# Optimization experiments

Hardware: AMD Instinct MI355X
Metric: run time of the kernel (lower is better)

The kernel has to match this reference:

```python
import jax, jax.numpy as jnp
import numpy as np
from jax import lax

NEG = -1e30  # finite stand-in for -inf (avoids NaN grads)
EPS = 1e-7   # keras backend epsilon used by ctc_batch_cost: log(y_pred + eps)

B, T, C, L = 64, 2048, 128, 256


def setup_inputs() -> dict:
    key = jax.random.key(0)
    k1, k2 = jax.random.split(key)
    # labels in [0, C-2]; blank index is C-1 per keras ctc_batch_cost convention
    y_true = jax.random.randint(k1, (B, L), 0, C - 1, dtype=jnp.int32).astype(jnp.int64)
    # y_pred are (unnormalized) per-frame class probabilities, as keras expects softmax output
    y_pred = jax.random.uniform(k2, (B, T, C), dtype=jnp.float32)
    return {"y_true": y_true, "y_pred": y_pred}


def _lse3(a, b, c):
    s = jnp.stack([a, b, c], axis=0)
    m = jnp.max(s, axis=0)
    return m + jnp.log(jnp.sum(jnp.exp(s - m), axis=0))


def _ctc_loss(y_true, y_pred):
    """Faithful jnp version of K.ctc_batch_cost with full input/label lengths."""
    b, t, c = y_pred.shape
    l = y_true.shape[1]
    blank = c - 1
    S = 2 * l + 1

    logp = jnp.log(y_pred + EPS)  # [B,T,C]

    labels = y_true.astype(jnp.int32)
    # extended label sequence: blank, l1, blank, l2, ..., blank  -> [B,S]
    ext = jnp.full((b, S), blank, dtype=jnp.int32).at[:, 1::2].set(labels)
    # gather per-frame log-probs of extended labels -> [B,T,S]
    lp_z = jnp.take_along_axis(logp, jnp.broadcast_to(ext[:, None, :], (b, t, S)), axis=2)

    # skip transition allowed at s if z[s] != blank and z[s] != z[s-2]
    ext_m2 = jnp.concatenate([jnp.full((b, 2), blank, jnp.int32), ext[:, :-2]], axis=1)
    skip = (ext != blank) & (ext != ext_m2) & (jnp.arange(S)[None, :] >= 2)  # [B,S]

    lp_tbs = jnp.transpose(lp_z, (1, 0, 2))  # [T,B,S]

    neg = jnp.full((b, S), NEG, dtype=logp.dtype)
    alpha0 = neg.at[:, 0].set(lp_tbs[0][:, 0]).at[:, 1].set(lp_tbs[0][:, 1])

    neg1 = jnp.full((b, 1), NEG, dtype=logp.dtype)
    neg2 = jnp.full((b, 2), NEG, dtype=logp.dtype)

    def step(alpha, lp_t):
        s1 = jnp.concatenate([neg1, alpha[:, :-1]], axis=1)
        s2 = jnp.where(skip, jnp.concatenate([neg2, alpha[:, :-2]], axis=1), NEG)
        new = _lse3(alpha, s1, s2) + lp_t
        return new, None

    alphaT, _ = lax.scan(step, alpha0, lp_tbs[1:])
    loss = -jnp.logaddexp(alphaT[:, -1], alphaT[:, -2])  # [B]
    return loss[:, None]  # keras ctc_batch_cost returns [B,1]


def reference(y_true, y_pred):
    return _ctc_loss(y_true, y_pred)
```

## Files before the change

### kernel.cpp

```cpp
#include <hip/hip_runtime.h>


#define B_ 64
#define T_ 2048
#define C_ 128
#define L_ 256
#define BLANK_ (C_ - 1)
#define EPSF 1e-7f
#define LN2F 0.69314718055994530942f
#define CH_ 16
#define NCHH_ 64
#define SENT_ (-(1 << 28))

typedef __attribute__((address_space(1))) const void glob_cv;
typedef __attribute__((address_space(3))) void lds_v;

__device__ __forceinline__ void gl2lds16(const float* g, float* l) {
    __builtin_amdgcn_global_load_lds((glob_cv*)g, (lds_v*)l, 16, 0, 0);
}

#define WAIT_VM(n) asm volatile("s_waitcnt vmcnt(" #n ")" ::: "memory")

__device__ __forceinline__ float dpp_shr1_f(float x) {
    return __int_as_float(
        __builtin_amdgcn_update_dpp(0, __float_as_int(x), 0x138, 0xf, 0xf, false));
}
__device__ __forceinline__ int dpp_shr1_i(int x) {
    return __builtin_amdgcn_update_dpp(0, x, 0x138, 0xf, 0xf, false);
}
__device__ __forceinline__ float dpp_shl1_f(float x) {
    return __int_as_float(
        __builtin_amdgcn_update_dpp(0, __float_as_int(x), 0x130, 0xf, 0xf, false));
}
__device__ __forceinline__ int dpp_shl1_i(int x) {
    return __builtin_amdgcn_update_dpp(0, x, 0x130, 0xf, 0xf, false);
}

struct G { float pb, p1, p3, p5, p7; };

__launch_bounds__(128, 1)
__global__ void ctc_loss_kernel(const int* __restrict__ y_true,
                                const float* __restrict__ y_pred,
                                float* __restrict__ out) {
    const int b = blockIdx.x;
    const int tid = threadIdx.x;
    const int w = __builtin_amdgcn_readfirstlane(tid >> 6);
    const int l = tid & 63;

    __shared__ float ring[2][4][CH_ * C_];

    const int* __restrict__ lab = y_true + b * L_;
    const int4 lv = *(const int4*)(lab + 4 * l);
    const int e1 = lv.x, e3 = lv.y, e5 = lv.z, e7 = lv.w;
    const int em1 = (l > 0) ? lab[4 * l - 1] : -1;
    const float m1f = ((l > 0) && (e1 != em1)) ? 1.0f : 0.0f;
    const float m3f = (e3 != e1) ? 1.0f : 0.0f;
    const float m5f = (e5 != e3) ? 1.0f : 0.0f;
    const float m7f = (e7 != e5) ? 1.0f : 0.0f;
    const float m8f = (l == 63) ? 1.0f : 0.0f;

    const float* __restrict__ base = y_pred + (size_t)b * (T_ * C_);

    float* __restrict__ rb = &ring[w][0][0];
    const float* __restrict__ cB = rb + BLANK_;
    const float* __restrict__ c1 = rb + e1;
    const float* __restrict__ c3 = rb + e3;
    const float* __restrict__ c5 = rb + e5;
    const float* __restrict__ c7 = rb + e7;

    auto issue_chunk = [&](int t0, int buf) {
        const float* g = base + (size_t)t0 * C_ + 4 * l;
        float* d = &ring[w][buf][0];
#pragma unroll
        for (int i = 0; i < 8; ++i)
            gl2lds16(g + i * 256, d + i * 256);
    };

    G g[4];
    auto fill = [&](int slot, int off) {
        g[slot].pb = cB[off] + EPSF;
        g[slot].p1 = c1[off] + EPSF;
        g[slot].p3 = c3[off] + EPSF;
        g[slot].p5 = c5[off] + EPSF;
        g[slot].p7 = c7[off] + EPSF;
    };

    float a0 = 0.f, a1 = 0.f, a2 = 0.f, a3 = 0.f, a4 = 0.f,
          a5 = 0.f, a6 = 0.f, a7 = 0.f, a8 = 0.f;
    int E = SENT_;
    float upscale = 1.0f;

    auto step = [&](const G& q) {
        const float up = dpp_shr1_f(a7) * upscale;
        const float n0 = (a0 + up) * q.pb;
        const float n1 = fmaf(m1f, up, a0 + a1) * q.p1;
        const float n2 = (a1 + a2) * q.pb;
        const float n3 = fmaf(m3f, a1, a2 + a3) * q.p3;
        const float n4 = (a3 + a4) * q.pb;
        const float n5 = fmaf(m5f, a3, a4 + a5) * q.p5;
        const float n6 = (a5 + a6) * q.pb;
        const float n7 = fmaf(m7f, a5, a6 + a7) * q.p7;
        const float n8 = fmaf(m8f, a7, a8) * q.pb;
        a0 = n0; a1 = n1; a2 = n2; a3 = n3; a4 = n4;
        a5 = n5; a6 = n6; a7 = n7; a8 = n8;
    };

    auto boundary = [&]() {
        float mx = fmaxf(fmaxf(fmaxf(a0, a1), fmaxf(a2, a3)),
                         fmaxf(fmaxf(a4, a5), fmaxf(a6, a7)));
        mx = fmaxf(mx, a8);
        const bool z = (mx == 0.0f);
        const int e = (int)(__float_as_uint(mx) >> 23) - 127;
        const float s = z ? 1.0f : __uint_as_float((unsigned)(127 - e) << 23);
        a0 *= s; a1 *= s; a2 *= s; a3 *= s; a4 *= s;
        a5 *= s; a6 *= s; a7 *= s; a8 *= s;
        E = z ? SENT_ : (E + e);
        int upE = dpp_shr1_i(E);
        if (l == 0) upE = SENT_;
        if (E == SENT_) E = upE;
        int d = upE - E;
        d = min(max(d, -126), 120);
        upscale = __uint_as_float((unsigned)(d + 127) << 23);
    };

    auto run_chunk = [&](int bc, int bn, int jstart, bool last) {
#pragma unroll
        for (int j = 0; j < CH_; ++j) {
            if (j == 0 && jstart) continue;
            step(g[j & 3]);
            if (!last || j < 12) {
                const int off = (j < 12) ? (bc * 2048 + (j + 4) * 128)
                                         : (bn * 2048 + (j - 12) * 128);
                fill(j & 3, off);
            }
            if ((j & 3) == 3) boundary();
        }
    };

    auto stepb = [&](const G& q) {
        const float d0 = a0 * q.pb, d1 = a1 * q.p1, d2 = a2 * q.pb,
                    d3 = a3 * q.p3, d4 = a4 * q.pb, d5 = a5 * q.p5,
                    d6 = a6 * q.pb, d7 = a7 * q.p7, d8 = a8 * q.pb;
        const float u = fmaf(m1f, d1, d0);
        const float dn = dpp_shl1_f(u) * upscale;
        a0 = d0 + d1;
        a1 = fmaf(m3f, d3, d1 + d2);
        a2 = d2 + d3;
        a3 = fmaf(m5f, d5, d3 + d4);
        a4 = d4 + d5;
        a5 = fmaf(m7f, d7, d5 + d6);
        a6 = d6 + d7;
        a7 = fmaf(m8f, d8, d7 + dn);
        a8 = d8;
    };

    auto boundaryb = [&]() {
        float mx = fmaxf(fmaxf(fmaxf(a0, a1), fmaxf(a2, a3)),
                         fmaxf(fmaxf(a4, a5), fmaxf(a6, a7)));
        mx = fmaxf(mx, a8);
        const bool z = (mx == 0.0f);
        const int e = (int)(__float_as_uint(mx) >> 23) - 127;
        const float s = z ? 1.0f : __uint_as_float((unsigned)(127 - e) << 23);
        a0 *= s; a1 *= s; a2 *= s; a3 *= s; a4 *= s;
        a5 *= s; a6 *= s; a7 *= s; a8 *= s;
        E = z ? SENT_ : (E + e);
        int upE = dpp_shl1_i(E);
        if (l == 63) upE = SENT_;
        if (E == SENT_) E = upE;
        int d = upE - E;
        d = min(max(d, -126), 120);
        upscale = __uint_as_float((unsigned)(d + 127) << 23);
    };

    auto run_chunkb = [&](int bc, int bn, bool last) {
#pragma unroll
        for (int j = 0; j < CH_; ++j) {
            stepb(g[j & 3]);
            if (!last || j < 12) {
                const int off = (j < 12) ? (bc * 2048 + (11 - j) * 128)
                                         : (bn * 2048 + (27 - j) * 128);
                fill(j & 3, off);
            }
            if ((j & 3) == 3) boundaryb();
        }
    };

    if (w == 0) {
        issue_chunk(0, 0);
        issue_chunk(CH_, 1);
        issue_chunk(2 * CH_, 2);

        WAIT_VM(8);
        issue_chunk(3 * CH_, 3);
        if (l == 0) { a0 = rb[BLANK_] + EPSF; a1 = rb[e1] + EPSF; E = 0; }
        boundary();
        fill(1, 1 * 128);
        fill(2, 2 * 128);
        fill(3, 3 * 128);
        fill(0, 4 * 128);
        run_chunk(0, 1, 1, false);
        WAIT_VM(8); issue_chunk(4 * CH_, 0); run_chunk(1, 2, 0, false);
        WAIT_VM(8); issue_chunk(5 * CH_, 1); run_chunk(2, 3, 0, false);
        WAIT_VM(8); issue_chunk(6 * CH_, 2); run_chunk(3, 0, 0, false);

        for (int m = 1; m <= 14; ++m) {
            const int c = 4 * m;
            WAIT_VM(8); issue_chunk((c + 3) * CH_, 3); run_chunk(0, 1, 0, false);
            WAIT_VM(8); issue_chunk((c + 4) * CH_, 0); run_chunk(1, 2, 0, false);
            WAIT_VM(8); issue_chunk((c + 5) * CH_, 1); run_chunk(2, 3, 0, false);
            WAIT_VM(8); issue_chunk((c + 6) * CH_, 2); run_chunk(3, 0, 0, false);
        }

        WAIT_VM(8); issue_chunk(63 * CH_, 3); run_chunk(0, 1, 0, false);
        WAIT_VM(8);
        run_chunk(1, 2, 0, false);
        WAIT_VM(0);
        run_chunk(2, 3, 0, false);
        run_chunk(3, 3, 0, true);
    } else {
        auto issq = [&](int q, int buf) { issue_chunk((127 - q) * CH_, buf); };
        issq(0, 0); issq(1, 1); issq(2, 2);

        WAIT_VM(8);
        issq(3, 3);
        if (l == 63) { a7 = 1.0f; a8 = 1.0f; E = 0; }
        boundaryb();
        fill(0, 15 * 128);
        fill(1, 14 * 128);
        fill(2, 13 * 128);
        fill(3, 12 * 128);
        run_chunkb(0, 1, false);
        WAIT_VM(8); issq(4, 0); run_chunkb(1, 2, false);
        WAIT_VM(8); issq(5, 1); run_chunkb(2, 3, false);
        WAIT_VM(8); issq(6, 2); run_chunkb(3, 0, false);

        for (int m = 1; m <= 14; ++m) {
            const int c = 4 * m;
            WAIT_VM(8); issq(c + 3, 3); run_chunkb(0, 1, false);
            WAIT_VM(8); issq(c + 4, 0); run_chunkb(1, 2, false);
            WAIT_VM(8); issq(c + 5, 1); run_chunkb(2, 3, false);
            WAIT_VM(8); issq(c + 6, 2); run_chunkb(3, 0, false);
        }

        WAIT_VM(8); issq(63, 3); run_chunkb(0, 1, false);
        WAIT_VM(8);
        run_chunkb(1, 2, false);
        WAIT_VM(0);
        run_chunkb(2, 3, false);
        run_chunkb(3, 3, true);
        float* xf = &ring[1][0][0];
        xf[0 * 64 + l] = a0; xf[1 * 64 + l] = a1; xf[2 * 64 + l] = a2;
        xf[3 * 64 + l] = a3; xf[4 * 64 + l] = a4; xf[5 * 64 + l] = a5;
        xf[6 * 64 + l] = a6; xf[7 * 64 + l] = a7; xf[8 * 64 + l] = a8;
        ((int*)xf)[9 * 64 + l] = E;
    }

    __syncthreads();

    if (w == 0) {
        const float* xf = &ring[1][0][0];
        float sd = a0 * xf[0 * 64 + l];
        sd = fmaf(a1, xf[1 * 64 + l], sd);
        sd = fmaf(a2, xf[2 * 64 + l], sd);
        sd = fmaf(a3, xf[3 * 64 + l], sd);
        sd = fmaf(a4, xf[4 * 64 + l], sd);
        sd = fmaf(a5, xf[5 * 64 + l], sd);
        sd = fmaf(a6, xf[6 * 64 + l], sd);
        sd = fmaf(a7, xf[7 * 64 + l], sd);
        sd = fmaf(a8, xf[8 * 64 + l], sd);
        const int E2 = ((const int*)xf)[9 * 64 + l];
        const bool nz = (sd > 0.0f);
        int Es = nz ? (E + E2) : SENT_;
        int M = Es;
#pragma unroll
        for (int o = 32; o; o >>= 1) M = max(M, __shfl_xor(M, o));
        int d = Es - M;
        d = max(d, -126);
        float val = nz ? sd * __uint_as_float((unsigned)(d + 127) << 23) : 0.0f;
#pragma unroll
        for (int o = 32; o; o >>= 1) val += __shfl_xor(val, o);
        if (l == 0) out[b] = -(__logf(val) + (float)M * LN2F);
    }
}

extern "C" void kernel_launch(void* const* d_in, const int* in_sizes, int n_in,
                              void* d_out, int out_size, void* d_ws, size_t ws_size,
                              hipStream_t stream) {
    const int* y_true = (const int*)d_in[0];
    const float* y_pred = (const float*)d_in[1];
    float* out = (float*)d_out;
    ctc_loss_kernel<<<B_, 128, 0, stream>>>(y_true, y_pred, out);
}
```

Baseline: 177.3 us.

## Replace fully unrolled chunk schedule with rolled 4-step group loops and rotating LDS offsets

The fully unrolled per-chunk pipeline, which expanded the whole time loop into straight-line code, becomes small rolled loops over 4-step groups. A running byte offset into a 32 KB LDS ring per wave replaces the fixed buffer indices. The backward wave stores each chunk in reversed row order so its fills use simple k^1 row offsets, and the EPS add moves from the fill into the step. The aim is to shrink code size and instruction-cache pressure, at the cost of loop overhead and offset arithmetic on the serial recurrence path.

```diff
diff --git a/kernel.cpp b/kernel.cpp
--- a/kernel.cpp
+++ b/kernel.cpp
@@ -9,13 +9,12 @@
 #define EPSF 1e-7f
 #define LN2F 0.69314718055994530942f
 #define CH_ 16
-#define NCHH_ 64
 #define SENT_ (-(1 << 28))
 
 typedef __attribute__((address_space(1))) const void glob_cv;
 typedef __attribute__((address_space(3))) void lds_v;
 
-__device__ __forceinline__ void gl2lds16(const float* g, float* l) {
+__device__ __forceinline__ void gl2lds16(const void* g, void* l) {
     __builtin_amdgcn_global_load_lds((glob_cv*)g, (lds_v*)l, 16, 0, 0);
 }
 
@@ -47,7 +46,7 @@
     const int w = __builtin_amdgcn_readfirstlane(tid >> 6);
     const int l = tid & 63;
 
-    __shared__ float ring[2][4][CH_ * C_];
+    __shared__ float ring[2][8192];
 
     const int* __restrict__ lab = y_true + b * L_;
     const int4 lv = *(const int4*)(lab + 4 * l);
@@ -61,46 +60,47 @@
 
     const float* __restrict__ base = y_pred + (size_t)b * (T_ * C_);
 
-    float* __restrict__ rb = &ring[w][0][0];
-    const float* __restrict__ cB = rb + BLANK_;
-    const float* __restrict__ c1 = rb + e1;
-    const float* __restrict__ c3 = rb + e3;
-    const float* __restrict__ c5 = rb + e5;
-    const float* __restrict__ c7 = rb + e7;
-
-    auto issue_chunk = [&](int t0, int buf) {
-        const float* g = base + (size_t)t0 * C_ + 4 * l;
-        float* d = &ring[w][buf][0];
-#pragma unroll
-        for (int i = 0; i < 8; ++i)
-            gl2lds16(g + i * 256, d + i * 256);
-    };
+    char* const lds0 = (char*)&ring[0][0];
+    const int rbase = w * 32768;
+    const int cBo = rbase + BLANK_ * 4;
+    const int c1o = rbase + e1 * 4;
+    const int c3o = rbase + e3 * 4;
+    const int c5o = rbase + e5 * 4;
+    const int c7o = rbase + e7 * 4;
+
+#define LDF(o) (*(const float*)(lds0 + (o)))
 
     G g[4];
-    auto fill = [&](int slot, int off) {
-        g[slot].pb = cB[off] + EPSF;
-        g[slot].p1 = c1[off] + EPSF;
-        g[slot].p3 = c3[off] + EPSF;
-        g[slot].p5 = c5[off] + EPSF;
-        g[slot].p7 = c7[off] + EPSF;
-    };
-
     float a0 = 0.f, a1 = 0.f, a2 = 0.f, a3 = 0.f, a4 = 0.f,
           a5 = 0.f, a6 = 0.f, a7 = 0.f, a8 = 0.f;
     int E = SENT_;
     float upscale = 1.0f;
+    int roff = 0;
+    int ldso = 0;
+    const char* gptr;
+
+    auto fillRow = [&](int slot, int row) {
+        const int ro = row * 512;
+        g[slot].pb = LDF(cBo + ro);
+        g[slot].p1 = LDF(c1o + ro);
+        g[slot].p3 = LDF(c3o + ro);
+        g[slot].p5 = LDF(c5o + ro);
+        g[slot].p7 = LDF(c7o + ro);
+    };
 
     auto step = [&](const G& q) {
+        const float pb = q.pb + EPSF, p1 = q.p1 + EPSF, p3 = q.p3 + EPSF,
+                    p5 = q.p5 + EPSF, p7 = q.p7 + EPSF;
         const float up = dpp_shr1_f(a7) * upscale;
-        const float n0 = (a0 + up) * q.pb;
-        const float n1 = fmaf(m1f, up, a0 + a1) * q.p1;
-        const float n2 = (a1 + a2) * q.pb;
-        const float n3 = fmaf(m3f, a1, a2 + a3) * q.p3;
-        const float n4 = (a3 + a4) * q.pb;
-        const float n5 = fmaf(m5f, a3, a4 + a5) * q.p5;
-        const float n6 = (a5 + a6) * q.pb;
-        const float n7 = fmaf(m7f, a5, a6 + a7) * q.p7;
-        const float n8 = fmaf(m8f, a7, a8) * q.pb;
+        const float n0 = (a0 + up) * pb;
+        const float n1 = fmaf(m1f, up, a0 + a1) * p1;
+        const float n2 = (a1 + a2) * pb;
+        const float n3 = fmaf(m3f, a1, a2 + a3) * p3;
+        const float n4 = (a3 + a4) * pb;
+        const float n5 = fmaf(m5f, a3, a4 + a5) * p5;
+        const float n6 = (a5 + a6) * pb;
+        const float n7 = fmaf(m7f, a5, a6 + a7) * p7;
+        const float n8 = fmaf(m8f, a7, a8) * pb;
         a0 = n0; a1 = n1; a2 = n2; a3 = n3; a4 = n4;
         a5 = n5; a6 = n6; a7 = n7; a8 = n8;
     };
@@ -123,24 +123,30 @@
         upscale = __uint_as_float((unsigned)(d + 127) << 23);
     };
 
-    auto run_chunk = [&](int bc, int bn, int jstart, bool last) {
-#pragma unroll
-        for (int j = 0; j < CH_; ++j) {
-            if (j == 0 && jstart) continue;
-            step(g[j & 3]);
-            if (!last || j < 12) {
-                const int off = (j < 12) ? (bc * 2048 + (j + 4) * 128)
-                                         : (bn * 2048 + (j - 12) * 128);
-                fill(j & 3, off);
+    auto grpF = [&](bool dofill) {
+        roff = (roff + 2048) & 32767;
+        const int oB = cBo + roff, o1 = c1o + roff, o3 = c3o + roff,
+                  o5 = c5o + roff, o7 = c7o + roff;
+#pragma unroll
+        for (int k = 0; k < 4; ++k) {
+            step(g[k]);
+            if (dofill) {
+                g[k].pb = LDF(oB + k * 512);
+                g[k].p1 = LDF(o1 + k * 512);
+                g[k].p3 = LDF(o3 + k * 512);
+                g[k].p5 = LDF(o5 + k * 512);
+                g[k].p7 = LDF(o7 + k * 512);
             }
-            if ((j & 3) == 3) boundary();
         }
+        boundary();
     };
 
     auto stepb = [&](const G& q) {
-        const float d0 = a0 * q.pb, d1 = a1 * q.p1, d2 = a2 * q.pb,
-                    d3 = a3 * q.p3, d4 = a4 * q.pb, d5 = a5 * q.p5,
-                    d6 = a6 * q.pb, d7 = a7 * q.p7, d8 = a8 * q.pb;
+        const float pb = q.pb + EPSF, p1 = q.p1 + EPSF, p3 = q.p3 + EPSF,
+                    p5 = q.p5 + EPSF, p7 = q.p7 + EPSF;
+        const float d0 = a0 * pb, d1 = a1 * p1, d2 = a2 * pb,
+                    d3 = a3 * p3, d4 = a4 * pb, d5 = a5 * p5,
+                    d6 = a6 * pb, d7 = a7 * p7, d8 = a8 * pb;
         const float u = fmaf(m1f, d1, d0);
         const float dn = dpp_shl1_f(u) * upscale;
         a0 = d0 + d1;
@@ -172,83 +178,99 @@
         upscale = __uint_as_float((unsigned)(d + 127) << 23);
     };
 
-    auto run_chunkb = [&](int bc, int bn, bool last) {
-#pragma unroll
-        for (int j = 0; j < CH_; ++j) {
-            stepb(g[j & 3]);
-            if (!last || j < 12) {
-                const int off = (j < 12) ? (bc * 2048 + (11 - j) * 128)
-                                         : (bn * 2048 + (27 - j) * 128);
-                fill(j & 3, off);
+    auto grpB = [&](bool dofill) {
+        roff = (roff + 2048) & 32767;
+        const int oB = cBo + roff, o1 = c1o + roff, o3 = c3o + roff,
+                  o5 = c5o + roff, o7 = c7o + roff;
+#pragma unroll
+        for (int k = 0; k < 4; ++k) {
+            stepb(g[k]);
+            if (dofill) {
+                const int ro = (k ^ 1) * 512;
+                g[k].pb = LDF(oB + ro);
+                g[k].p1 = LDF(o1 + ro);
+                g[k].p3 = LDF(o3 + ro);
+                g[k].p5 = LDF(o5 + ro);
+                g[k].p7 = LDF(o7 + ro);
             }
-            if ((j & 3) == 3) boundaryb();
         }
+        boundaryb();
+    };
+
+    auto issueF = [&]() {
+#pragma unroll
+        for (int i = 0; i < 8; ++i)
+            gl2lds16(gptr + i * 1024, lds0 + rbase + ldso + i * 1024);
+        gptr += 8192;
+        ldso = (ldso + 8192) & 32767;
+    };
+    auto issueB = [&]() {
+#pragma unroll
+        for (int i = 0; i < 8; ++i)
+            gl2lds16(gptr + i * 1024, lds0 + rbase + ldso + (7168 - i * 1024));
+        gptr -= 8192;
+        ldso = (ldso + 8192) & 32767;
     };
 
     if (w == 0) {
-        issue_chunk(0, 0);
-        issue_chunk(CH_, 1);
-        issue_chunk(2 * CH_, 2);
-
+        gptr = (const char*)(base + 4 * l);
+        issueF(); issueF(); issueF();
         WAIT_VM(8);
-        issue_chunk(3 * CH_, 3);
-        if (l == 0) { a0 = rb[BLANK_] + EPSF; a1 = rb[e1] + EPSF; E = 0; }
+        issueF();
+        if (l == 0) { a0 = LDF(cBo) + EPSF; a1 = LDF(c1o) + EPSF; E = 0; }
         boundary();
-        fill(1, 1 * 128);
-        fill(2, 2 * 128);
-        fill(3, 3 * 128);
-        fill(0, 4 * 128);
-        run_chunk(0, 1, 1, false);
-        WAIT_VM(8); issue_chunk(4 * CH_, 0); run_chunk(1, 2, 0, false);
-        WAIT_VM(8); issue_chunk(5 * CH_, 1); run_chunk(2, 3, 0, false);
-        WAIT_VM(8); issue_chunk(6 * CH_, 2); run_chunk(3, 0, 0, false);
-
-        for (int m = 1; m <= 14; ++m) {
-            const int c = 4 * m;
-            WAIT_VM(8); issue_chunk((c + 3) * CH_, 3); run_chunk(0, 1, 0, false);
-            WAIT_VM(8); issue_chunk((c + 4) * CH_, 0); run_chunk(1, 2, 0, false);
-            WAIT_VM(8); issue_chunk((c + 5) * CH_, 1); run_chunk(2, 3, 0, false);
-            WAIT_VM(8); issue_chunk((c + 6) * CH_, 2); run_chunk(3, 0, 0, false);
+        fillRow(1, 1); fillRow(2, 2); fillRow(3, 3); fillRow(0, 4);
+        step(g[1]); fillRow(1, 5);
+        step(g[2]); fillRow(2, 6);
+        step(g[3]); fillRow(3, 7);
+        boundary();
+        roff = 2048;
+#pragma unroll 1
+        for (int gg = 0; gg < 3; ++gg) grpF(true);
+#pragma unroll 1
+        for (int c = 1; c <= 60; ++c) {
+            WAIT_VM(8);
+            issueF();
+#pragma unroll 1
+            for (int gg = 0; gg < 4; ++gg) grpF(true);
         }
-
-        WAIT_VM(8); issue_chunk(63 * CH_, 3); run_chunk(0, 1, 0, false);
         WAIT_VM(8);
-        run_chunk(1, 2, 0, false);
+#pragma unroll 1
+        for (int gg = 0; gg < 4; ++gg) grpF(true);
         WAIT_VM(0);
-        run_chunk(2, 3, 0, false);
-        run_chunk(3, 3, 0, true);
+#pragma unroll 1
+        for (int gg = 0; gg < 4; ++gg) grpF(true);
+#pragma unroll 1
+        for (int gg = 0; gg < 3; ++gg) grpF(true);
+        grpF(false);
     } else {
-        auto issq = [&](int q, int buf) { issue_chunk((127 - q) * CH_, buf); };
-        issq(0, 0); issq(1, 1); issq(2, 2);
-
+        gptr = (const char*)(base + 127 * CH_ * C_ + 4 * l);
+        issueB(); issueB(); issueB();
         WAIT_VM(8);
-        issq(3, 3);
+        issueB();
         if (l == 63) { a7 = 1.0f; a8 = 1.0f; E = 0; }
         boundaryb();
-        fill(0, 15 * 128);
-        fill(1, 14 * 128);
-        fill(2, 13 * 128);
-        fill(3, 12 * 128);
-        run_chunkb(0, 1, false);
-        WAIT_VM(8); issq(4, 0); run_chunkb(1, 2, false);
-        WAIT_VM(8); issq(5, 1); run_chunkb(2, 3, false);
-        WAIT_VM(8); issq(6, 2); run_chunkb(3, 0, false);
-
-        for (int m = 1; m <= 14; ++m) {
-            const int c = 4 * m;
-            WAIT_VM(8); issq(c + 3, 3); run_chunkb(0, 1, false);
-            WAIT_VM(8); issq(c + 4, 0); run_chunkb(1, 2, false);
-            WAIT_VM(8); issq(c + 5, 1); run_chunkb(2, 3, false);
-            WAIT_VM(8); issq(c + 6, 2); run_chunkb(3, 0, false);
+        fillRow(0, 1); fillRow(1, 0); fillRow(2, 3); fillRow(3, 2);
+        roff = 0;
+#pragma unroll 1
+        for (int gg = 0; gg < 4; ++gg) grpB(true);
+#pragma unroll 1
+        for (int c = 1; c <= 60; ++c) {
+            WAIT_VM(8);
+            issueB();
+#pragma unroll 1
+            for (int gg = 0; gg < 4; ++gg) grpB(true);
         }
-
-        WAIT_VM(8); issq(63, 3); run_chunkb(0, 1, false);
         WAIT_VM(8);
-        run_chunkb(1, 2, false);
+#pragma unroll 1
+        for (int gg = 0; gg < 4; ++gg) grpB(true);
         WAIT_VM(0);
-        run_chunkb(2, 3, false);
-        run_chunkb(3, 3, true);
-        float* xf = &ring[1][0][0];
+#pragma unroll 1
+        for (int gg = 0; gg < 4; ++gg) grpB(true);
+#pragma unroll 1
+        for (int gg = 0; gg < 3; ++gg) grpB(true);
+        grpB(false);
+        float* xf = &ring[1][0];
         xf[0 * 64 + l] = a0; xf[1 * 64 + l] = a1; xf[2 * 64 + l] = a2;
         xf[3 * 64 + l] = a3; xf[4 * 64 + l] = a4; xf[5 * 64 + l] = a5;
         xf[6 * 64 + l] = a6; xf[7 * 64 + l] = a7; xf[8 * 64 + l] = a8;
@@ -258,7 +280,7 @@
     __syncthreads();
 
     if (w == 0) {
-        const float* xf = &ring[1][0][0];
+        const float* xf = &ring[1][0];
         float sd = a0 * xf[0 * 64 + l];
         sd = fmaf(a1, xf[1 * 64 + l], sd);
         sd = fmaf(a2, xf[2 * 64 + l], sd);
```

Result: slower. 181.6 us (+2.4%).
